# Kernel tuning notes

Hardware: AMD Instinct MI355X
Metric: run time of the kernel (lower is better)

The kernel has to match this reference:

```python
import jax, jax.numpy as jnp
import numpy as np

B, N, D, H = 64, 64, 128, 256
DIN = N + 4        # z_where(2) + one-hot(N) + actions(2)
DOUT = 2
TAU = 0.5
BN_EPS = 1e-5
KL_EPS = 1e-16


def mlp_bn(x, w1, b1, g, bb, w2, b2):
    # Linear -> ReLU -> BatchNorm1d (training mode, stats over all leading dims) -> Linear
    h = jax.nn.relu(jnp.einsum('...i,ih->...h', x, w1) + b1)
    hf = h.reshape(-1, h.shape[-1])
    mu = hf.mean(0)
    var = hf.var(0)  # biased variance, as torch BN uses for normalization
    h = (h - mu) * jax.lax.rsqrt(var + BN_EPS) * g + bb
    return jnp.einsum('...h,ho->...o', h, w2) + b2


def setup_inputs():
    key = jax.random.key(0)
    ks = jax.random.split(key, 16)
    def W(k, i, o):
        return jax.random.normal(k, (i, o), jnp.float32) / np.float32(np.sqrt(i))
    u = jax.random.uniform(ks[0], (B, N, N, 2), jnp.float32, 1e-10, 1.0 - 1e-10)
    gumbel_noise = -jnp.log(-jnp.log(u))
    z = jnp.zeros
    return {
        'states': jax.random.normal(ks[1], (B, N, D), jnp.float32),
        'z_where': jax.random.normal(ks[2], (B, N, 2), jnp.float32),
        'actions': jax.random.normal(ks[3], (B, 2), jnp.float32),
        'gumbel_noise': gumbel_noise,
        'self_w1': W(ks[4], DIN, H), 'self_b1': z((H,)), 'self_g': jnp.ones((H,)), 'self_bb': z((H,)),
        'self_w2': W(ks[5], H, D), 'self_b2': z((D,)),
        'rel_w1': W(ks[6], 2 * D, H), 'rel_b1': z((H,)), 'rel_g': jnp.ones((H,)), 'rel_bb': z((H,)),
        'rel_w2': W(ks[7], H, D), 'rel_b2': z((D,)),
        'wgt_w1': W(ks[8], 2 * D, H), 'wgt_b1': z((H,)), 'wgt_g': jnp.ones((H,)), 'wgt_bb': z((H,)),
        'wgt_w2': W(ks[9], H, 2), 'wgt_b2': z((2,)),
        'pred_w1': W(ks[10], D, H), 'pred_b1': z((H,)), 'pred_g': jnp.ones((H,)), 'pred_bb': z((H,)),
        'pred_w2': W(ks[11], H, DOUT), 'pred_b2': z((DOUT,)),
        'gru_wih': W(ks[12], 2 * D, 3 * D), 'gru_whh': W(ks[13], D, 3 * D),
        'gru_bih': z((3 * D,)), 'gru_bhh': z((3 * D,)),
    }


def prop_gt_forward(states, z_where, actions, gumbel_noise,
                    self_w1, self_b1, self_g, self_bb, self_w2, self_b2,
                    rel_w1, rel_b1, rel_g, rel_bb, rel_w2, rel_b2,
                    wgt_w1, wgt_b1, wgt_g, wgt_bb, wgt_w2, wgt_b2,
                    pred_w1, pred_b1, pred_g, pred_bb, pred_w2, pred_b2,
                    gru_wih, gru_whh, gru_bih, gru_bhh):
    b = states.shape[0]
    eye = jnp.eye(N, dtype=states.dtype)
    # feat = [z_where, one-hot id, broadcast action] : (B, N, DIN)
    z_what = jnp.broadcast_to(eye[None], (b, N, N))
    act = jnp.broadcast_to(actions[:, None, :], (b, N, 2))
    feat = jnp.concatenate([z_where, z_what, act], axis=-1)
    enc_self = mlp_bn(feat, self_w1, self_b1, self_g, self_bb, self_w2, self_b2)  # (B,N,D)

    # recurrent dynamics: pairwise state concat (B, N, N, 2D)
    s_self = jnp.broadcast_to(states[:, :, None, :], (b, N, N, D))
    s_other = jnp.broadcast_to(states[:, None, :, :], (b, N, N, D))
    feat_matrix = jnp.concatenate([s_self, s_other], axis=-1)

    relational = mlp_bn(feat_matrix, rel_w1, rel_b1, rel_g, rel_bb, rel_w2, rel_b2)  # (B,N,N,D)
    logits = mlp_bn(feat_matrix, wgt_w1, wgt_b1, wgt_g, wgt_bb, wgt_w2, wgt_b2)      # (B,N,N,2)

    # gumbel-softmax, hard with straight-through
    y_soft = jax.nn.softmax((logits + gumbel_noise) / TAU, axis=-1)
    y_hard = jax.nn.one_hot(jnp.argmax(y_soft, axis=-1), 2, dtype=y_soft.dtype)
    y = jax.lax.stop_gradient(y_hard - y_soft) + y_soft
    weight = y[..., 0:1]  # (B,N,N,1)

    # KL(prob || prior) as in NRI
    log_prior = jnp.log(jnp.array([0.05, 0.95], dtype=logits.dtype))
    prob = jax.nn.softmax(logits, axis=-1)
    kl_loss = jnp.sum(prob * (jnp.log(prob + KL_EPS) - log_prior)) / (N * b)

    # self mask: zero diagonal edges
    weight = weight * (1.0 - eye)[None, :, :, None]

    enc_rel = jnp.sum(weight * relational, axis=2)  # (B,N,D)

    # TrackerRNN: GRU cell update of states with [enc_self, enc_rel]
    x = jnp.concatenate([enc_self, enc_rel], axis=-1)  # (B,N,2D)
    gi = jnp.einsum('bni,ih->bnh', x, gru_wih) + gru_bih
    gh = jnp.einsum('bnd,dh->bnh', states, gru_whh) + gru_bhh
    gi_r, gi_z, gi_n = jnp.split(gi, 3, axis=-1)
    gh_r, gh_z, gh_n = jnp.split(gh, 3, axis=-1)
    r = jax.nn.sigmoid(gi_r + gh_r)
    zg = jax.nn.sigmoid(gi_z + gh_z)
    n = jnp.tanh(gi_n + r * gh_n)
    updated_state = (1.0 - zg) * n + zg * states  # (B,N,D)

    z_where_next = mlp_bn(updated_state, pred_w1, pred_b1, pred_g, pred_bb, pred_w2, pred_b2)
    return (updated_state, z_where_next.reshape(b, -1), weight, kl_loss)


def reference(states, z_where, actions, gumbel_noise,
              self_w1, self_b1, self_g, self_bb, self_w2, self_b2,
              rel_w1, rel_b1, rel_g, rel_bb, rel_w2, rel_b2,
              wgt_w1, wgt_b1, wgt_g, wgt_bb, wgt_w2, wgt_b2,
              pred_w1, pred_b1, pred_g, pred_bb, pred_w2, pred_b2,
              gru_wih, gru_whh, gru_bih, gru_bhh):
    return prop_gt_forward(states, z_where, actions, gumbel_noise,
                           self_w1, self_b1, self_g, self_bb, self_w2, self_b2,
                           rel_w1, rel_b1, rel_g, rel_bb, rel_w2, rel_b2,
                           wgt_w1, wgt_b1, wgt_g, wgt_bb, wgt_w2, wgt_b2,
                           pred_w1, pred_b1, pred_g, pred_bb, pred_w2, pred_b2,
                           gru_wih, gru_whh, gru_bih, gru_bhh)
```

## Files before the change

kernel.cpp:

```cpp
#include <hip/hip_runtime.h>
#include <math.h>

#define BATCH 64
#define NOBJ  64
#define DDIM  128
#define HDIM  256
#define ROWS  (BATCH*NOBJ)
#define PAIRS (ROWS*NOBJ)

#define OFF_A_REL    (0ull)
#define OFF_B_REL    (4ull<<20)
#define OFF_A_WGT    (8ull<<20)
#define OFF_B_WGT    (12ull<<20)
#define OFF_BWT      (16ull<<20)
#define OFF_H_SELF   (20ull<<20)
#define OFF_ENC_SELF (24ull<<20)
#define OFF_ENC_REL  (26ull<<20)
#define OFF_H_PRED   (28ull<<20)
#define OFF_STATS    (32ull<<20)
#define OFF_KLP      (OFF_STATS + 16384)
#define OFF_W2P      (OFF_STATS + 65536)
#define OFF_C2       (OFF_W2P + 128*1024)
#define OFF_W2PD     (OFF_C2 + 512)
#define OFF_C2W      (OFF_W2PD + 4096)
#define OFF_SW2P     (OFF_C2W + 256)
#define OFF_SC2      (OFF_SW2P + 128*1024)

#define OUT_UPD 0
#define OUT_ZWN (ROWS*DDIM)
#define OUT_WGT (OUT_ZWN + ROWS*2)
#define OUT_KL  (OUT_WGT + PAIRS)

__global__ __launch_bounds__(256) void k_zero(double* __restrict__ p)
{
    p[blockIdx.x*256 + threadIdx.x] = 0.0;
}

__global__ __launch_bounds__(256) void k_pre(
    const float* __restrict__ states,
    const float* __restrict__ rel_w1, const float* __restrict__ rel_b1,
    const float* __restrict__ wgt_w1, const float* __restrict__ wgt_b1,
    const float* __restrict__ z_where, const float* __restrict__ actions,
    const float* __restrict__ self_w1, const float* __restrict__ self_b1,
    float* __restrict__ A_rel, float* __restrict__ B_rel,
    float* __restrict__ A_wgt, float* __restrict__ B_wgt,
    float* __restrict__ B_wgtT, float* __restrict__ h_self,
    double* __restrict__ stats)
{
    const int t = threadIdx.x;
    const int view = blockIdx.y;

    if (view == 2) {
        if (blockIdx.x >= 256) return;
        const int row0 = blockIdx.x * 16;
        const float w_zw0 = self_w1[0*256+t], w_zw1 = self_w1[1*256+t];
        const float w_a0  = self_w1[66*256+t], w_a1 = self_w1[67*256+t];
        const float bb1 = self_b1[t];
        double sum = 0.0, ssq = 0.0;
        for (int r = 0; r < 16; ++r) {
            const int row = row0 + r;
            const int b = row >> 6, i = row & 63;
            const float zw0 = z_where[row*2], zw1 = z_where[row*2+1];
            const float a0 = actions[b*2], a1 = actions[b*2+1];
            float v = self_w1[(2+i)*256+t] + bb1;
            v = fmaf(zw0, w_zw0, v); v = fmaf(zw1, w_zw1, v);
            v = fmaf(a0, w_a0, v);   v = fmaf(a1, w_a1, v);
            v = fmaxf(v, 0.f);
            h_self[row*256+t] = v;
            sum += (double)v; ssq = fma((double)v, (double)v, ssq);
        }
        atomicAdd(&stats[4*256+t], sum);
        atomicAdd(&stats[5*256+t], ssq);
        return;
    }

    const int row0 = blockIdx.x * 8;
    __shared__ float s_tile[8][128];
    for (int f4 = t; f4 < 256; f4 += 256)
        *(float4*)&s_tile[0][f4*4] = *(const float4*)&states[row0*128 + f4*4];
    __syncthreads();

    const float* wbase = (view == 0) ? rel_w1 : wgt_w1;
    const float* wpA = wbase + t;
    const float* wpB = wbase + 128*256 + t;
    float accA[8], accB[8];
#pragma unroll
    for (int r = 0; r < 8; ++r) { accA[r] = 0.f; accB[r] = 0.f; }
#pragma unroll 4
    for (int k = 0; k < 128; ++k) {
        const float wvA = wpA[k*256];
        const float wvB = wpB[k*256];
#pragma unroll
        for (int r = 0; r < 8; ++r) {
            const float s = s_tile[r][k];
            accA[r] = fmaf(s, wvA, accA[r]);
            accB[r] = fmaf(s, wvB, accB[r]);
        }
    }

    if (view == 0) {
        const float bias = rel_b1[t];
#pragma unroll
        for (int r = 0; r < 8; ++r) {
            A_rel[(row0+r)*256 + t] = accA[r] + bias;
            B_rel[(row0+r)*256 + t] = accB[r];
        }
    } else {
        const float bias = wgt_b1[t];
#pragma unroll
        for (int r = 0; r < 8; ++r) {
            A_wgt[(row0+r)*256 + t] = accA[r] + bias;
            B_wgt[(row0+r)*256 + t] = accB[r];
        }
        const int b = row0 >> 6, j0 = row0 & 63;
        float* bt = &B_wgtT[((size_t)b*256 + t)*64 + j0];
        *(float4*)(bt+0) = make_float4(accB[0], accB[1], accB[2], accB[3]);
        *(float4*)(bt+4) = make_float4(accB[4], accB[5], accB[6], accB[7]);
    }
}

__global__ __launch_bounds__(256) void k_bn_stats(
    const float* __restrict__ A_rel, const float* __restrict__ B_rel,
    const float* __restrict__ A_wgt, const float* __restrict__ B_wgt,
    double* __restrict__ stats)
{
    const int h = threadIdx.x;
    const int b = blockIdx.y, i0 = blockIdx.x * 8;
    float ar[8], aw[8];
#pragma unroll
    for (int r = 0; r < 8; ++r) {
        ar[r] = A_rel[(b*64 + i0 + r)*256 + h];
        aw[r] = A_wgt[(b*64 + i0 + r)*256 + h];
    }
    float  srel0 = 0.f, ssrel0 = 0.f, srel1 = 0.f, ssrel1 = 0.f;
    double swgt = 0.0, sswgt = 0.0;
    for (int j = 0; j < 64; j += 2) {
        const float br0 = B_rel[(b*64+j)*256 + h];
        const float bw0 = B_wgt[(b*64+j)*256 + h];
        const float br1 = B_rel[(b*64+j+1)*256 + h];
        const float bw1 = B_wgt[(b*64+j+1)*256 + h];
#pragma unroll
        for (int r = 0; r < 8; ++r) {
            const float v0 = fmaxf(ar[r] + br0, 0.f);
            srel0 += v0; ssrel0 = fmaf(v0, v0, ssrel0);
            const float vw0 = fmaxf(aw[r] + bw0, 0.f);
            swgt += (double)vw0; sswgt = fma((double)vw0, (double)vw0, sswgt);
        }
#pragma unroll
        for (int r = 0; r < 8; ++r) {
            const float v1 = fmaxf(ar[r] + br1, 0.f);
            srel1 += v1; ssrel1 = fmaf(v1, v1, ssrel1);
            const float vw1 = fmaxf(aw[r] + bw1, 0.f);
            swgt += (double)vw1; sswgt = fma((double)vw1, (double)vw1, sswgt);
        }
    }
    atomicAdd(&stats[0*256+h], (double)(srel0 + srel1));
    atomicAdd(&stats[1*256+h], (double)(ssrel0 + ssrel1));
    atomicAdd(&stats[2*256+h], swgt);
    atomicAdd(&stats[3*256+h], sswgt);
}

__global__ __launch_bounds__(256) void k_finalize(
    const double* __restrict__ stats,
    const float* __restrict__ rel_g, const float* __restrict__ rel_bb,
    const float* __restrict__ rel_w2, const float* __restrict__ rel_b2,
    const float* __restrict__ wgt_g, const float* __restrict__ wgt_bb,
    const float* __restrict__ wgt_w2, const float* __restrict__ wgt_b2,
    const float* __restrict__ self_g, const float* __restrict__ self_bb,
    const float* __restrict__ self_w2, const float* __restrict__ self_b2,
    float* __restrict__ W2p, float* __restrict__ c2,
    double* __restrict__ W2pd, double* __restrict__ c2w,
    float* __restrict__ sW2p, float* __restrict__ sc2)
{
    __shared__ float  rscale[256], rshift[256], sscale[256], sshift[256];
    __shared__ double wshift[256];
    const int k = threadIdx.x;
    {
        const double cnt = 262144.0;
        double mu  = stats[0*256+k]/cnt;
        double var = stats[1*256+k]/cnt - mu*mu;
        float  sc  = (float)((double)rel_g[k] / sqrt(var + 1e-5));
        rscale[k] = sc;
        rshift[k] = rel_bb[k] - (float)mu * sc;
        double muw  = stats[2*256+k]/cnt;
        double varw = stats[3*256+k]/cnt - muw*muw;
        double scw  = (double)wgt_g[k] / sqrt(varw + 1e-5);
        wshift[k]   = (double)wgt_bb[k] - muw*scw;
        if (blockIdx.x == 0) {
            W2pd[2*k]   = scw * (double)wgt_w2[2*k];
            W2pd[2*k+1] = scw * (double)wgt_w2[2*k+1];
        }
        const double cnts = 4096.0;
        double mus  = stats[4*256+k]/cnts;
        double vars = stats[5*256+k]/cnts - mus*mus;
        float  scs  = (float)((double)self_g[k] / sqrt(vars + 1e-5));
        sscale[k] = scs;
        sshift[k] = self_bb[k] - (float)mus*scs;
    }
    __syncthreads();
    const int base = blockIdx.x * 8192;
    for (int idx = base + k; idx < base + 8192; idx += 256) {
        const int kk = idx >> 7;
        W2p[idx]  = rscale[kk]*rel_w2[idx];
        sW2p[idx] = sscale[kk]*self_w2[idx];
    }
    if (blockIdx.x == 0) {
        if (k < 128) {
            float acc = rel_b2[k], accs = self_b2[k];
            for (int kk = 0; kk < 256; ++kk) {
                acc  = fmaf(rshift[kk], rel_w2[kk*128+k], acc);
                accs = fmaf(sshift[kk], self_w2[kk*128+k], accs);
            }
            c2[k] = acc; sc2[k] = accs;
        }
        if (k < 2) {
            double acc = (double)wgt_b2[k];
            for (int kk = 0; kk < 256; ++kk) acc += wshift[kk]*(double)wgt_w2[kk*2+k];
            c2w[k] = acc;
        }
    }
}

__global__ __launch_bounds__(256) void k_main(
    const float* __restrict__ A_rel, const float* __restrict__ B_rel,
    const float* __restrict__ A_wgt, const float* __restrict__ B_wgtT,
    const double* __restrict__ W2pd, const double* __restrict__ c2w,
    const float* __restrict__ gumbel,
    const float* __restrict__ W2p, const float* __restrict__ c2,
    float* __restrict__ enc_rel, float* __restrict__ weight_out,
    float* __restrict__ klp)
{
    __shared__ float  a_lds[4][256];
    __shared__ double w2_lds[512];
    __shared__ double red0[4][4][64], red1[4][4][64];
    __shared__ float  w_lds[4][64];
    __shared__ float  klred[256];
    __shared__ float  h_lds[4][256];
    __shared__ float  redf[4][256];
    const int t = threadIdx.x;
    const int blk = blockIdx.x;
    const int row0 = blk * 4;
    const int b = row0 >> 6;

    w2_lds[t]     = W2pd[t];
    w2_lds[256+t] = W2pd[256+t];
    float a_rel[4];
#pragma unroll
    for (int r = 0; r < 4; ++r) {
        a_lds[r][t] = A_wgt[(row0+r)*256 + t];
        a_rel[r]    = A_rel[(row0+r)*256 + t];
    }
    __syncthreads();

    {
        const int j = t & 63, q = t >> 6;
        double acc0[4] = {0,0,0,0}, acc1[4] = {0,0,0,0};
        const float* btp = &B_wgtT[((size_t)b*256 + q*64)*64 + j];
#pragma unroll 4
        for (int kk = 0; kk < 64; ++kk) {
            const int k = q*64 + kk;
            const float  bw = btp[kk*64];
            const double w0 = w2_lds[2*k], w1 = w2_lds[2*k+1];
#pragma unroll
            for (int r = 0; r < 4; ++r) {
                const double hw = (double)fmaxf(a_lds[r][k] + bw, 0.f);
                acc0[r] = fma(hw, w0, acc0[r]);
                acc1[r] = fma(hw, w1, acc1[r]);
            }
        }
#pragma unroll
        for (int r = 0; r < 4; ++r) { red0[r][q][j] = acc0[r]; red1[r][q][j] = acc1[r]; }
    }
    __syncthreads();

    {
        const int r = t >> 6, j = t & 63;
        const double l0 = red0[r][0][j]+red0[r][1][j]+red0[r][2][j]+red0[r][3][j] + c2w[0];
        const double l1 = red1[r][0][j]+red1[r][1][j]+red1[r][2][j]+red1[r][3][j] + c2w[1];
        const int row = row0 + r;
        const float g0 = gumbel[(row*64+j)*2], g1 = gumbel[(row*64+j)*2+1];
        float w = (l0 + (double)g0 >= l1 + (double)g1) ? 1.f : 0.f;
        if (j == (row & 63)) w = 0.f;
        w_lds[r][j] = w;
        weight_out[row*64 + j] = w;
        const float lf0 = (float)l0, lf1 = (float)l1;
        const float m = fmaxf(lf0, lf1);
        const float e0 = expf(lf0 - m), e1 = expf(lf1 - m);
        const float s = e0 + e1;
        const float p0 = e0/s, p1 = e1/s;
        const float lp0 = -2.9957323f;
        const float lp1 = -0.05129329f;
        klred[t] = p0*(logf(p0+1e-16f) - lp0) + p1*(logf(p1+1e-16f) - lp1);
    }
    __syncthreads();
    if (t < 64) {
        float s = klred[t] + klred[t+64] + klred[t+128] + klred[t+192];
        for (int off = 32; off; off >>= 1) s += __shfl_down(s, off);
        if (t == 0) klp[blk] = s;
    }

    float sumw[4] = {0,0,0,0};
    {
        float g[4] = {0,0,0,0};
#pragma unroll 4
        for (int j = 0; j < 64; ++j) {
            const float br = B_rel[(b*64+j)*256 + t];
#pragma unroll
            for (int r = 0; r < 4; ++r) {
                const float w = w_lds[r][j];
                sumw[r] += w;
                g[r] = fmaf(w, fmaxf(a_rel[r] + br, 0.f), g[r]);
            }
        }
#pragma unroll
        for (int r = 0; r < 4; ++r) h_lds[r][t] = g[r];
    }
    __syncthreads();
    {
        const int d = t & 127, half = t >> 7;
        float acc[4] = {0,0,0,0};
        const float* wp = &W2p[half*128*128 + d];
#pragma unroll 2
        for (int kk = 0; kk < 128; ++kk) {
            const float wv = wp[kk*128];
#pragma unroll
            for (int r = 0; r < 4; ++r)
                acc[r] = fmaf(h_lds[r][half*128 + kk], wv, acc[r]);
        }
#pragma unroll
        for (int r = 0; r < 4; ++r) redf[r][t] = acc[r];
    }
    __syncthreads();
    if (t < 128) {
#pragma unroll
        for (int r = 0; r < 4; ++r)
            enc_rel[(row0+r)*128 + t] = redf[r][t] + redf[r][t+128] + sumw[r]*c2[t];
    }
}

__global__ __launch_bounds__(256) void k_enc_self(
    const float* __restrict__ h_self, const float* __restrict__ sW2p,
    const float* __restrict__ sc2, float* __restrict__ enc_self)
{
    __shared__ float h_lds[16*256];
    const int t = threadIdx.x;
    const int row0 = blockIdx.x * 16;
    for (int f4 = t; f4 < 1024; f4 += 256)
        *(float4*)&h_lds[f4*4] = *(const float4*)&h_self[row0*256 + f4*4];
    __syncthreads();
    const int d = t & 127, half = t >> 7;
    float acc[16];
#pragma unroll
    for (int r = 0; r < 16; ++r) acc[r] = 0.f;
    for (int kk = 0; kk < 128; ++kk) {
        const int k = half*128 + kk;
        const float wv = sW2p[k*128 + d];
#pragma unroll
        for (int r = 0; r < 16; ++r) acc[r] = fmaf(h_lds[r*256 + k], wv, acc[r]);
    }
    __syncthreads();
#pragma unroll
    for (int r = 0; r < 16; ++r) h_lds[r*256 + t] = acc[r];
    __syncthreads();
    for (int idx = t; idx < 16*128; idx += 256) {
        const int r = idx >> 7, dd = idx & 127;
        enc_self[(row0+r)*128 + dd] = h_lds[r*256 + dd] + h_lds[r*256 + 128 + dd] + sc2[dd];
    }
}

__global__ __launch_bounds__(192) void k_gru(
    const float* __restrict__ enc_self, const float* __restrict__ enc_rel,
    const float* __restrict__ states,
    const float* __restrict__ wih, const float* __restrict__ whh,
    const float* __restrict__ bih, const float* __restrict__ bhh,
    float* __restrict__ updated)
{
    __shared__ float x_lds[4][256];
    __shared__ float s_lds[4][128];
    __shared__ float gi_lds[4][384];
    __shared__ float gh_lds[4][384];
    const int t = threadIdx.x;
    const int row0 = blockIdx.x * 4;
    for (int idx = t; idx < 4*256; idx += 192) {
        const int r = idx >> 8, k = idx & 255;
        x_lds[r][k] = (k < 128) ? enc_self[(row0+r)*128 + k]
                                : enc_rel[(row0+r)*128 + (k-128)];
    }
    for (int idx = t; idx < 4*128; idx += 192) {
        const int r = idx >> 7, k = idx & 127;
        s_lds[r][k] = states[(row0+r)*128 + k];
    }
    __syncthreads();
    const int c0 = t, c1 = t + 192;
    float gi0[4], gh0[4], gi1[4], gh1[4];
    const float bi0 = bih[c0], bh0 = bhh[c0];
    const float bi1 = bih[c1], bh1 = bhh[c1];
#pragma unroll
    for (int r = 0; r < 4; ++r) { gi0[r] = bi0; gh0[r] = bh0; gi1[r] = bi1; gh1[r] = bh1; }

    for (int k0 = 0; k0 < 128; k0 += 4) {
        float4 xv[4], sv[4];
#pragma unroll
        for (int r = 0; r < 4; ++r) {
            xv[r] = *(const float4*)&x_lds[r][k0];
            sv[r] = *(const float4*)&s_lds[r][k0];
        }
        float wi0[4], wi1[4], wh0[4], wh1[4];
#pragma unroll
        for (int kk = 0; kk < 4; ++kk) {
            wi0[kk] = wih[(k0+kk)*384 + c0];
            wi1[kk] = wih[(k0+kk)*384 + c1];
            wh0[kk] = whh[(k0+kk)*384 + c0];
            wh1[kk] = whh[(k0+kk)*384 + c1];
        }
#pragma unroll
        for (int kk = 0; kk < 4; ++kk) {
#pragma unroll
            for (int r = 0; r < 4; ++r) {
                const float x = ((const float*)&xv[r])[kk];
                const float s = ((const float*)&sv[r])[kk];
                gi0[r] = fmaf(x, wi0[kk], gi0[r]);
                gi1[r] = fmaf(x, wi1[kk], gi1[r]);
                gh0[r] = fmaf(s, wh0[kk], gh0[r]);
                gh1[r] = fmaf(s, wh1[kk], gh1[r]);
            }
        }
    }
    for (int k0 = 128; k0 < 256; k0 += 4) {
        float4 xv[4];
#pragma unroll
        for (int r = 0; r < 4; ++r)
            xv[r] = *(const float4*)&x_lds[r][k0];
        float wi0[4], wi1[4];
#pragma unroll
        for (int kk = 0; kk < 4; ++kk) {
            wi0[kk] = wih[(k0+kk)*384 + c0];
            wi1[kk] = wih[(k0+kk)*384 + c1];
        }
#pragma unroll
        for (int kk = 0; kk < 4; ++kk) {
#pragma unroll
            for (int r = 0; r < 4; ++r) {
                const float x = ((const float*)&xv[r])[kk];
                gi0[r] = fmaf(x, wi0[kk], gi0[r]);
                gi1[r] = fmaf(x, wi1[kk], gi1[r]);
            }
        }
    }
#pragma unroll
    for (int r = 0; r < 4; ++r) {
        gi_lds[r][c0] = gi0[r]; gi_lds[r][c1] = gi1[r];
        gh_lds[r][c0] = gh0[r]; gh_lds[r][c1] = gh1[r];
    }
    __syncthreads();
    for (int idx = t; idx < 4*128; idx += 192) {
        const int r = idx >> 7, d = idx & 127;
        const float gr = gi_lds[r][d]       + gh_lds[r][d];
        const float gz = gi_lds[r][128+d]   + gh_lds[r][128+d];
        const float rr = 1.f/(1.f + expf(-gr));
        const float zz = 1.f/(1.f + expf(-gz));
        const float nn = tanhf(gi_lds[r][256+d] + rr*gh_lds[r][256+d]);
        updated[(row0+r)*128 + d] = (1.f - zz)*nn + zz*s_lds[r][d];
    }
}

__global__ __launch_bounds__(256) void k_pred_h(
    const float* __restrict__ updated, const float* __restrict__ w1,
    const float* __restrict__ b1, float* __restrict__ h_pred,
    double* __restrict__ stats)
{
    __shared__ float u_lds[16][128];
    const int h = threadIdx.x;
    const int row0 = blockIdx.x * 16;
    for (int f4 = h; f4 < 512; f4 += 256)
        *(float4*)&u_lds[0][f4*4] = *(const float4*)&updated[row0*128 + f4*4];
    __syncthreads();
    float acc[16];
    const float bb1 = b1[h];
#pragma unroll
    for (int r = 0; r < 16; ++r) acc[r] = bb1;
#pragma unroll 4
    for (int k = 0; k < 128; ++k) {
        const float w = w1[k*256 + h];
#pragma unroll
        for (int r = 0; r < 16; ++r) acc[r] = fmaf(u_lds[r][k], w, acc[r]);
    }
    double sum = 0.0, ssq = 0.0;
#pragma unroll
    for (int r = 0; r < 16; ++r) {
        const float v = fmaxf(acc[r], 0.f);
        h_pred[(row0+r)*256 + h] = v;
        sum += (double)v; ssq = fma((double)v, (double)v, ssq);
    }
    atomicAdd(&stats[6*256+h], sum);
    atomicAdd(&stats[7*256+h], ssq);
}

__global__ __launch_bounds__(256) void k_pred_out(
    const float* __restrict__ h_pred, const double* __restrict__ stats,
    const float* __restrict__ g, const float* __restrict__ bbv,
    const float* __restrict__ w2, const float* __restrict__ b2,
    const float* __restrict__ klp,
    float* __restrict__ out_zw, float* __restrict__ out_kl)
{
    __shared__ float scale_lds[256], shift_lds[256];
    __shared__ float h_lds[32*256];
    __shared__ float red0[256], red1[256];
    __shared__ double kred[4];
    const int t = threadIdx.x;
    {
        const double mu  = stats[6*256+t]/4096.0;
        const double var = stats[7*256+t]/4096.0 - mu*mu;
        const float  sc  = (float)((double)g[t]/sqrt(var + 1e-5));
        scale_lds[t] = sc;
        shift_lds[t] = bbv[t] - (float)mu*sc;
    }
    const int row0 = blockIdx.x * 32;
    for (int idx = t; idx < 32*256; idx += 256)
        h_lds[idx] = h_pred[row0*256 + idx];
    __syncthreads();
    const int rl = t >> 3, q = t & 7;
    float a0 = 0.f, a1 = 0.f;
    for (int kk = 0; kk < 32; ++kk) {
        const int k = q*32 + kk;
        const float hn = fmaf(h_lds[rl*256 + k], scale_lds[k], shift_lds[k]);
        a0 = fmaf(hn, w2[k*2],   a0);
        a1 = fmaf(hn, w2[k*2+1], a1);
    }
    red0[t] = a0; red1[t] = a1;
    __syncthreads();
    if (t < 32) {
        float z0 = b2[0], z1 = b2[1];
        for (int q2 = 0; q2 < 8; ++q2) { z0 += red0[t*8+q2]; z1 += red1[t*8+q2]; }
        out_zw[(row0+t)*2]   = z0;
        out_zw[(row0+t)*2+1] = z1;
    }
    if (blockIdx.x == 0) {
        double s = 0.0;
        for (int idx = t; idx < 1024; idx += 256) s += (double)klp[idx];
        for (int off = 32; off; off >>= 1) s += __shfl_down(s, off);
        if ((t & 63) == 0) kred[t >> 6] = s;
        __syncthreads();
        if (t == 0)
            out_kl[0] = (float)((kred[0]+kred[1]+kred[2]+kred[3]) / 4096.0);
    }
}

extern "C" void kernel_launch(void* const* d_in, const int* in_sizes, int n_in,
                              void* d_out, int out_size, void* d_ws, size_t ws_size,
                              hipStream_t stream) {
    const float* states   = (const float*)d_in[0];
    const float* z_where  = (const float*)d_in[1];
    const float* actions  = (const float*)d_in[2];
    const float* gumbel   = (const float*)d_in[3];
    const float* self_w1  = (const float*)d_in[4];
    const float* self_b1  = (const float*)d_in[5];
    const float* self_g   = (const float*)d_in[6];
    const float* self_bb  = (const float*)d_in[7];
    const float* self_w2  = (const float*)d_in[8];
    const float* self_b2  = (const float*)d_in[9];
    const float* rel_w1   = (const float*)d_in[10];
    const float* rel_b1   = (const float*)d_in[11];
    const float* rel_g    = (const float*)d_in[12];
    const float* rel_bb   = (const float*)d_in[13];
    const float* rel_w2   = (const float*)d_in[14];
    const float* rel_b2   = (const float*)d_in[15];
    const float* wgt_w1   = (const float*)d_in[16];
    const float* wgt_b1   = (const float*)d_in[17];
    const float* wgt_g    = (const float*)d_in[18];
    const float* wgt_bb   = (const float*)d_in[19];
    const float* wgt_w2   = (const float*)d_in[20];
    const float* wgt_b2   = (const float*)d_in[21];
    const float* pred_w1  = (const float*)d_in[22];
    const float* pred_b1  = (const float*)d_in[23];
    const float* pred_g   = (const float*)d_in[24];
    const float* pred_bb  = (const float*)d_in[25];
    const float* pred_w2  = (const float*)d_in[26];
    const float* pred_b2  = (const float*)d_in[27];
    const float* gru_wih  = (const float*)d_in[28];
    const float* gru_whh  = (const float*)d_in[29];
    const float* gru_bih  = (const float*)d_in[30];
    const float* gru_bhh  = (const float*)d_in[31];

    char* ws = (char*)d_ws;
    float*  A_rel  = (float*) (ws + OFF_A_REL);
    float*  B_rel  = (float*) (ws + OFF_B_REL);
    float*  A_wgt  = (float*) (ws + OFF_A_WGT);
    float*  B_wgt  = (float*) (ws + OFF_B_WGT);
    float*  B_wgtT = (float*) (ws + OFF_BWT);
    float*  h_self = (float*) (ws + OFF_H_SELF);
    float*  encS   = (float*) (ws + OFF_ENC_SELF);
    float*  encR   = (float*) (ws + OFF_ENC_REL);
    float*  h_pred = (float*) (ws + OFF_H_PRED);
    double* stats  = (double*)(ws + OFF_STATS);
    float*  klp    = (float*) (ws + OFF_KLP);
    float*  W2p    = (float*) (ws + OFF_W2P);
    float*  c2     = (float*) (ws + OFF_C2);
    double* W2pd   = (double*)(ws + OFF_W2PD);
    double* c2w    = (double*)(ws + OFF_C2W);
    float*  sW2p   = (float*) (ws + OFF_SW2P);
    float*  sc2    = (float*) (ws + OFF_SC2);

    float* out = (float*)d_out;

    k_zero<<<8, 256, 0, stream>>>(stats);
    k_pre<<<dim3(512, 3), 256, 0, stream>>>(states, rel_w1, rel_b1, wgt_w1, wgt_b1,
                                            z_where, actions, self_w1, self_b1,
                                            A_rel, B_rel, A_wgt, B_wgt, B_wgtT,
                                            h_self, stats);
    k_bn_stats<<<dim3(8, 64), 256, 0, stream>>>(A_rel, B_rel, A_wgt, B_wgt, stats);
    k_finalize<<<4, 256, 0, stream>>>(stats, rel_g, rel_bb, rel_w2, rel_b2,
                                      wgt_g, wgt_bb, wgt_w2, wgt_b2,
                                      self_g, self_bb, self_w2, self_b2,
                                      W2p, c2, W2pd, c2w, sW2p, sc2);
    k_main<<<1024, 256, 0, stream>>>(A_rel, B_rel, A_wgt, B_wgtT, W2pd, c2w,
                                     gumbel, W2p, c2, encR, out + OUT_WGT, klp);
    k_enc_self<<<256, 256, 0, stream>>>(h_self, sW2p, sc2, encS);
    k_gru<<<1024, 192, 0, stream>>>(encS, encR, states, gru_wih, gru_whh,
                                    gru_bih, gru_bhh, out + OUT_UPD);
    k_pred_h<<<256, 256, 0, stream>>>(out + OUT_UPD, pred_w1, pred_b1, h_pred, stats);
    k_pred_out<<<128, 256, 0, stream>>>(h_pred, stats, pred_g, pred_bb, pred_w2, pred_b2,
                                        klp, out + OUT_ZWN, out + OUT_KL);
}
```

Before: 195.6 us.

## Fuse self-encoder output, GRU and prediction hidden layer into one kernel

Folds the enc_self projection and the pred MLP first layer into the GRU kernel, so each 4-row block computes enc_self from h_self, runs the GRU, then computes h_pred from the updated state kept in LDS. This removes two kernel launches and the global round trips for enc_self and the updated state. In exchange, weights (sW2p, pred_w1) are re-read by 1024 blocks instead of 256, with only 4 rows of reuse per weight load. The stats atomics also rise from 256 to 1024 per hidden unit.

```diff
diff --git a/kernel.cpp b/kernel.cpp
--- a/kernel.cpp
+++ b/kernel.cpp
@@ -14,7 +14,6 @@
 #define OFF_B_WGT    (12ull<<20)
 #define OFF_BWT      (16ull<<20)
 #define OFF_H_SELF   (20ull<<20)
-#define OFF_ENC_SELF (24ull<<20)
 #define OFF_ENC_REL  (26ull<<20)
 #define OFF_H_PRED   (28ull<<20)
 #define OFF_STATS    (32ull<<20)
@@ -338,59 +337,45 @@
     }
 }
 
-__global__ __launch_bounds__(256) void k_enc_self(
+__global__ __launch_bounds__(192) void k_gru(
     const float* __restrict__ h_self, const float* __restrict__ sW2p,
-    const float* __restrict__ sc2, float* __restrict__ enc_self)
-{
-    __shared__ float h_lds[16*256];
-    const int t = threadIdx.x;
-    const int row0 = blockIdx.x * 16;
-    for (int f4 = t; f4 < 1024; f4 += 256)
-        *(float4*)&h_lds[f4*4] = *(const float4*)&h_self[row0*256 + f4*4];
-    __syncthreads();
-    const int d = t & 127, half = t >> 7;
-    float acc[16];
-#pragma unroll
-    for (int r = 0; r < 16; ++r) acc[r] = 0.f;
-    for (int kk = 0; kk < 128; ++kk) {
-        const int k = half*128 + kk;
-        const float wv = sW2p[k*128 + d];
-#pragma unroll
-        for (int r = 0; r < 16; ++r) acc[r] = fmaf(h_lds[r*256 + k], wv, acc[r]);
-    }
-    __syncthreads();
-#pragma unroll
-    for (int r = 0; r < 16; ++r) h_lds[r*256 + t] = acc[r];
-    __syncthreads();
-    for (int idx = t; idx < 16*128; idx += 256) {
-        const int r = idx >> 7, dd = idx & 127;
-        enc_self[(row0+r)*128 + dd] = h_lds[r*256 + dd] + h_lds[r*256 + 128 + dd] + sc2[dd];
-    }
-}
-
-__global__ __launch_bounds__(192) void k_gru(
-    const float* __restrict__ enc_self, const float* __restrict__ enc_rel,
-    const float* __restrict__ states,
+    const float* __restrict__ sc2,
+    const float* __restrict__ enc_rel, const float* __restrict__ states,
     const float* __restrict__ wih, const float* __restrict__ whh,
     const float* __restrict__ bih, const float* __restrict__ bhh,
-    float* __restrict__ updated)
+    const float* __restrict__ pred_w1, const float* __restrict__ pred_b1,
+    float* __restrict__ updated, float* __restrict__ h_pred,
+    double* __restrict__ stats)
 {
+    __shared__ float hs_lds[4][256];
     __shared__ float x_lds[4][256];
     __shared__ float s_lds[4][128];
     __shared__ float gi_lds[4][384];
     __shared__ float gh_lds[4][384];
     const int t = threadIdx.x;
     const int row0 = blockIdx.x * 4;
-    for (int idx = t; idx < 4*256; idx += 192) {
-        const int r = idx >> 8, k = idx & 255;
-        x_lds[r][k] = (k < 128) ? enc_self[(row0+r)*128 + k]
-                                : enc_rel[(row0+r)*128 + (k-128)];
-    }
+
+    for (int f4 = t; f4 < 256; f4 += 192)
+        *(float4*)&hs_lds[0][f4*4] = *(const float4*)&h_self[row0*256 + f4*4];
     for (int idx = t; idx < 4*128; idx += 192) {
         const int r = idx >> 7, k = idx & 127;
-        s_lds[r][k] = states[(row0+r)*128 + k];
-    }
-    __syncthreads();
+        s_lds[r][k]     = states[(row0+r)*128 + k];
+        x_lds[r][128+k] = enc_rel[(row0+r)*128 + k];
+    }
+    __syncthreads();
+
+    for (int idx = t; idx < 512; idx += 192) {
+        const int r = idx >> 7, d = idx & 127;
+        float lo = 0.f, hi = 0.f;
+#pragma unroll 4
+        for (int kk = 0; kk < 128; ++kk) {
+            lo = fmaf(hs_lds[r][kk],     sW2p[kk*128 + d],       lo);
+            hi = fmaf(hs_lds[r][128+kk], sW2p[(128+kk)*128 + d], hi);
+        }
+        x_lds[r][d] = lo + hi + sc2[d];
+    }
+    __syncthreads();
+
     const int c0 = t, c1 = t + 192;
     float gi0[4], gh0[4], gi1[4], gh1[4];
     const float bi0 = bih[c0], bh0 = bhh[c0];
@@ -460,40 +445,33 @@
         const float rr = 1.f/(1.f + expf(-gr));
         const float zz = 1.f/(1.f + expf(-gz));
         const float nn = tanhf(gi_lds[r][256+d] + rr*gh_lds[r][256+d]);
-        updated[(row0+r)*128 + d] = (1.f - zz)*nn + zz*s_lds[r][d];
-    }
-}
-
-__global__ __launch_bounds__(256) void k_pred_h(
-    const float* __restrict__ updated, const float* __restrict__ w1,
-    const float* __restrict__ b1, float* __restrict__ h_pred,
-    double* __restrict__ stats)
-{
-    __shared__ float u_lds[16][128];
-    const int h = threadIdx.x;
-    const int row0 = blockIdx.x * 16;
-    for (int f4 = h; f4 < 512; f4 += 256)
-        *(float4*)&u_lds[0][f4*4] = *(const float4*)&updated[row0*128 + f4*4];
-    __syncthreads();
-    float acc[16];
-    const float bb1 = b1[h];
-#pragma unroll
-    for (int r = 0; r < 16; ++r) acc[r] = bb1;
+        const float upd = (1.f - zz)*nn + zz*s_lds[r][d];
+        updated[(row0+r)*128 + d] = upd;
+        hs_lds[r][d] = upd;
+    }
+    __syncthreads();
+
+    for (int h = t; h < 256; h += 192) {
+        float acc[4];
+        const float bb1 = pred_b1[h];
+#pragma unroll
+        for (int r = 0; r < 4; ++r) acc[r] = bb1;
 #pragma unroll 4
-    for (int k = 0; k < 128; ++k) {
-        const float w = w1[k*256 + h];
-#pragma unroll
-        for (int r = 0; r < 16; ++r) acc[r] = fmaf(u_lds[r][k], w, acc[r]);
-    }
-    double sum = 0.0, ssq = 0.0;
-#pragma unroll
-    for (int r = 0; r < 16; ++r) {
-        const float v = fmaxf(acc[r], 0.f);
-        h_pred[(row0+r)*256 + h] = v;
-        sum += (double)v; ssq = fma((double)v, (double)v, ssq);
-    }
-    atomicAdd(&stats[6*256+h], sum);
-    atomicAdd(&stats[7*256+h], ssq);
+        for (int k = 0; k < 128; ++k) {
+            const float w = pred_w1[k*256 + h];
+#pragma unroll
+            for (int r = 0; r < 4; ++r) acc[r] = fmaf(hs_lds[r][k], w, acc[r]);
+        }
+        double sum = 0.0, ssq = 0.0;
+#pragma unroll
+        for (int r = 0; r < 4; ++r) {
+            const float v = fmaxf(acc[r], 0.f);
+            h_pred[(row0+r)*256 + h] = v;
+            sum += (double)v; ssq = fma((double)v, (double)v, ssq);
+        }
+        atomicAdd(&stats[6*256+h], sum);
+        atomicAdd(&stats[7*256+h], ssq);
+    }
 }
 
 __global__ __launch_bounds__(256) void k_pred_out(
@@ -589,7 +567,6 @@
     float*  B_wgt  = (float*) (ws + OFF_B_WGT);
     float*  B_wgtT = (float*) (ws + OFF_BWT);
     float*  h_self = (float*) (ws + OFF_H_SELF);
-    float*  encS   = (float*) (ws + OFF_ENC_SELF);
     float*  encR   = (float*) (ws + OFF_ENC_REL);
     float*  h_pred = (float*) (ws + OFF_H_PRED);
     double* stats  = (double*)(ws + OFF_STATS);
@@ -615,10 +592,10 @@
                                       W2p, c2, W2pd, c2w, sW2p, sc2);
     k_main<<<1024, 256, 0, stream>>>(A_rel, B_rel, A_wgt, B_wgtT, W2pd, c2w,
                                      gumbel, W2p, c2, encR, out + OUT_WGT, klp);
-    k_enc_self<<<256, 256, 0, stream>>>(h_self, sW2p, sc2, encS);
-    k_gru<<<1024, 192, 0, stream>>>(encS, encR, states, gru_wih, gru_whh,
-                                    gru_bih, gru_bhh, out + OUT_UPD);
-    k_pred_h<<<256, 256, 0, stream>>>(out + OUT_UPD, pred_w1, pred_b1, h_pred, stats);
+    k_gru<<<1024, 192, 0, stream>>>(h_self, sW2p, sc2, encR, states,
+                                    gru_wih, gru_whh, gru_bih, gru_bhh,
+                                    pred_w1, pred_b1,
+                                    out + OUT_UPD, h_pred, stats);
     k_pred_out<<<128, 256, 0, stream>>>(h_pred, stats, pred_g, pred_bb, pred_w2, pred_b2,
                                         klp, out + OUT_ZWN, out + OUT_KL);
 }
```

After: 213.3 us. +9.0%, slower.
